# Optimization experiments

Hardware: AMD Instinct MI355X
Metric: run time of the kernel (lower is better)

Reference implementation:

```python
import jax, jax.numpy as jnp
import numpy as np

HID = 4096      # hidden_size
H = 32          # num_attention_heads
K = 8           # num_key_value_heads
D = HID // H    # head_dim = 128
G = H // K      # q heads per kv group = 4
INTER = 14336   # intermediate_size
T = 2048        # tokens (prefill)
EPS = 1e-5
THETA = 1000000.0


def setup_inputs() -> dict:
    key = jax.random.key(0)
    ks = jax.random.split(key, 9)
    s = 0.02
    return {
        "hidden_states": jax.random.normal(ks[0], (T, HID), jnp.float32),
        "position_ids": jnp.arange(T, dtype=jnp.int64),
        "wqkv": jax.random.normal(ks[1], ((H + 2 * K) * D, HID), jnp.float32) * s,
        "wo": jax.random.normal(ks[2], (HID, HID), jnp.float32) * s,
        "w1": jax.random.normal(ks[3], (INTER, HID), jnp.float32) * s,  # gate
        "w3": jax.random.normal(ks[4], (INTER, HID), jnp.float32) * s,  # up
        "w2": jax.random.normal(ks[5], (HID, INTER), jnp.float32) * s,  # down
        "attn_norm_w": jnp.ones((HID,), jnp.float32),
        "ffn_norm_w": jnp.ones((HID,), jnp.float32),
    }


def _rmsnorm(x, w):
    var = jnp.mean(jnp.square(x), axis=-1, keepdims=True)
    return x * jax.lax.rsqrt(var + EPS) * w


def _rope(x, cos, sin):
    # non-interleaved (half-split) rotation; x: [T, h, D], cos/sin: [T, 1, D//2]
    x1, x2 = x[..., : D // 2], x[..., D // 2 :]
    return jnp.concatenate([x1 * cos - x2 * sin, x2 * cos + x1 * sin], axis=-1)


def _attention(x, position_ids, wqkv, wo):
    t = x.shape[0]
    qkv = x @ wqkv.T  # [T, (H+2K)*D]
    q = qkv[:, : H * D].reshape(t, H, D)
    k = qkv[:, H * D : (H + K) * D].reshape(t, K, D)
    v = qkv[:, (H + K) * D :].reshape(t, K, D)

    inv_freq = 1.0 / (THETA ** (jnp.arange(0, D, 2, dtype=jnp.float32) / D))
    freqs = position_ids.astype(jnp.float32)[:, None] * inv_freq  # [T, D//2]
    cos = jnp.cos(freqs)[:, None, :]
    sin = jnp.sin(freqs)[:, None, :]
    q = _rope(q, cos, sin)
    k = _rope(k, cos, sin)

    # grouped-query attention: [T, K, G, D] queries vs [T, K, D] keys
    qg = q.reshape(t, K, G, D)
    scale = 1.0 / jnp.sqrt(jnp.float32(D))
    scores = jnp.einsum("tkgd,skd->kgts", qg, k) * scale  # [K, G, T, T]
    causal = jnp.tril(jnp.ones((t, t), dtype=bool))
    scores = jnp.where(causal, scores, jnp.finfo(scores.dtype).min)
    probs = jax.nn.softmax(scores, axis=-1)
    out = jnp.einsum("kgts,skd->tkgd", probs, v).reshape(t, H * D)
    return out @ wo.T


def _mlp(x, w1, w3, w2):
    return (jax.nn.silu(x @ w1.T) * (x @ w3.T)) @ w2.T


def reference(hidden_states, position_ids, wqkv, wo, w1, w3, w2, attn_norm_w, ffn_norm_w):
    h = hidden_states + _attention(_rmsnorm(hidden_states, attn_norm_w), position_ids, wqkv, wo)
    return h + _mlp(_rmsnorm(h, ffn_norm_w), w1, w3, w2)
```

## Files before the change

### kernel.cpp

```cpp
#include <hip/hip_runtime.h>
#include <stdint.h>

#define T_SEQ 2048
#define HIDN  4096
#define NH    32
#define NKV   8
#define DH    128
#define INTER 14336
#define QKV_N 6144
#define EPSR  1e-5f
#define SCALE 0.08838834764831845f

typedef __bf16 bf16x8 __attribute__((ext_vector_type(8)));
typedef float  f32x4  __attribute__((ext_vector_type(4)));

__device__ __forceinline__ f32x4 mfma16(bf16x8 a, bf16x8 b, f32x4 c) {
  return __builtin_amdgcn_mfma_f32_16x16x32_bf16(a, b, c, 0, 0, 0);
}

__device__ __forceinline__ void glds16(const void* g, void* l) {
  __builtin_amdgcn_global_load_lds(
      (__attribute__((address_space(1))) void*)g,
      (__attribute__((address_space(3))) void*)l,
      16, 0, 0);
}

__global__ __launch_bounds__(256) void cvt_bf16_kernel(
    const float* __restrict__ src, __bf16* __restrict__ dst, long n) {
  long stride = (long)gridDim.x * 256 * 8;
  for (long i = ((long)blockIdx.x * 256 + threadIdx.x) * 8; i < n; i += stride) {
    float4 a = *(const float4*)(src + i);
    float4 b = *(const float4*)(src + i + 4);
    bf16x8 o;
    o[0]=(__bf16)a.x; o[1]=(__bf16)a.y; o[2]=(__bf16)a.z; o[3]=(__bf16)a.w;
    o[4]=(__bf16)b.x; o[5]=(__bf16)b.y; o[6]=(__bf16)b.z; o[7]=(__bf16)b.w;
    *(bf16x8*)(dst + i) = o;
  }
}

__global__ __launch_bounds__(256) void rmsnorm_kernel(
    const float* __restrict__ x, const float* __restrict__ w,
    __bf16* __restrict__ y) {
  const int row = blockIdx.x, tid = threadIdx.x;
  const float* xr = x + (size_t)row * HIDN + tid * 16;
  float4 v0 = ((const float4*)xr)[0];
  float4 v1 = ((const float4*)xr)[1];
  float4 v2 = ((const float4*)xr)[2];
  float4 v3 = ((const float4*)xr)[3];
  float ss = v0.x*v0.x + v0.y*v0.y + v0.z*v0.z + v0.w*v0.w
           + v1.x*v1.x + v1.y*v1.y + v1.z*v1.z + v1.w*v1.w
           + v2.x*v2.x + v2.y*v2.y + v2.z*v2.z + v2.w*v2.w
           + v3.x*v3.x + v3.y*v3.y + v3.z*v3.z + v3.w*v3.w;
  #pragma unroll
  for (int off = 32; off >= 1; off >>= 1) ss += __shfl_xor(ss, off, 64);
  __shared__ float red[4];
  if ((tid & 63) == 0) red[tid >> 6] = ss;
  __syncthreads();
  float rn = rsqrtf((red[0] + red[1] + red[2] + red[3]) * (1.0f / HIDN) + EPSR);
  const float* wr = w + tid * 16;
  float4 w0 = ((const float4*)wr)[0];
  float4 w1v = ((const float4*)wr)[1];
  float4 w2v = ((const float4*)wr)[2];
  float4 w3v = ((const float4*)wr)[3];
  bf16x8 o0, o1;
  o0[0]=(__bf16)(v0.x*rn*w0.x);  o0[1]=(__bf16)(v0.y*rn*w0.y);
  o0[2]=(__bf16)(v0.z*rn*w0.z);  o0[3]=(__bf16)(v0.w*rn*w0.w);
  o0[4]=(__bf16)(v1.x*rn*w1v.x); o0[5]=(__bf16)(v1.y*rn*w1v.y);
  o0[6]=(__bf16)(v1.z*rn*w1v.z); o0[7]=(__bf16)(v1.w*rn*w1v.w);
  o1[0]=(__bf16)(v2.x*rn*w2v.x); o1[1]=(__bf16)(v2.y*rn*w2v.y);
  o1[2]=(__bf16)(v2.z*rn*w2v.z); o1[3]=(__bf16)(v2.w*rn*w2v.w);
  o1[4]=(__bf16)(v3.x*rn*w3v.x); o1[5]=(__bf16)(v3.y*rn*w3v.y);
  o1[6]=(__bf16)(v3.z*rn*w3v.z); o1[7]=(__bf16)(v3.w*rn*w3v.w);
  __bf16* yo = y + (size_t)row * HIDN + tid * 16;
  *(bf16x8*)(yo)     = o0;
  *(bf16x8*)(yo + 8) = o1;
}

template<int EPI>
__global__ __launch_bounds__(512, 2) void gemm256_kernel(
    const __bf16* __restrict__ A, const __bf16* __restrict__ B,
    void* __restrict__ Cout, int M, int N, int Kfull, int KZ) {
  extern __shared__ __align__(16) char smem[];
  const int tid = threadIdx.x;
  const int lane = tid & 63;
  const int wv = tid >> 6;
  const int wm = wv >> 2;
  const int wn = wv & 3;
  const int lr = lane & 15, q = lane >> 4;

  const int gx = gridDim.x, gy = gridDim.y;
  const int nwg = gx * gy;
  const int orig = blockIdx.y * gx + blockIdx.x;
  const int cpx = nwg >> 3;
  const int swz = (orig & 7) * cpx + (orig >> 3);
  const int by = swz % gy, bx = swz / gy;
  const int m0 = by * 256, n0 = bx * 256;
  const int kbase = blockIdx.z * KZ;
  const int NT = KZ >> 5;

  const char* aS[2]; const char* bS[2]; int Lds[2];
  #pragma unroll
  for (int j = 0; j < 2; j++) {
    int L = j * 512 + tid;
    int row = L >> 2;
    int s = (L & 3) ^ ((row >> 1) & 3);
    aS[j] = (const char*)(A + (size_t)(m0 + row) * Kfull + kbase + s * 8);
    bS[j] = (const char*)(B + (size_t)(n0 + row) * Kfull + kbase + s * 8);
    Lds[j] = L * 16;
  }

  const int sA = q ^ ((lr >> 1) & 3);
  int aoff[8], boff[4];
  #pragma unroll
  for (int mt = 0; mt < 8; mt++) aoff[mt] = (wm * 128 + mt * 16 + lr) * 64 + sA * 16;
  #pragma unroll
  for (int nt = 0; nt < 4; nt++) boff[nt] = 16384 + (wn * 64 + nt * 16 + lr) * 64 + sA * 16;

#define STAGE_T(tile, sb) do {                                   \
    char* _b = smem + (sb) * 32768;                              \
    size_t _ko = (size_t)(tile) * 64;                            \
    glds16(aS[0] + _ko, _b + Lds[0]);                            \
    glds16(aS[1] + _ko, _b + Lds[1]);                            \
    glds16(bS[0] + _ko, _b + 16384 + Lds[0]);                    \
    glds16(bS[1] + _ko, _b + 16384 + Lds[1]);                    \
  } while (0)

#define GBODY(VMC, DOST) do {                                    \
    if (DOST) { STAGE_T(t + 3, sbufi); sbufi = (sbufi == 4) ? 0 : sbufi + 1; } \
    asm volatile("s_waitcnt vmcnt(" #VMC ")" ::: "memory");      \
    __builtin_amdgcn_s_barrier();                                \
    asm volatile("" ::: "memory");                               \
    __builtin_amdgcn_sched_barrier(0);                           \
    { const char* _bA = smem + bufi * 32768;                     \
      bf16x8 bf[4], af[8];                                       \
      _Pragma("unroll") for (int nt = 0; nt < 4; nt++)           \
        bf[nt] = *(const bf16x8*)(_bA + boff[nt]);               \
      _Pragma("unroll") for (int mt = 0; mt < 8; mt++)           \
        af[mt] = *(const bf16x8*)(_bA + aoff[mt]);               \
      __builtin_amdgcn_s_setprio(1);                             \
      _Pragma("unroll") for (int mt = 0; mt < 8; mt++)           \
        _Pragma("unroll") for (int nt = 0; nt < 4; nt++)         \
          acc[mt][nt] = mfma16(af[mt], bf[nt], acc[mt][nt]);     \
      __builtin_amdgcn_s_setprio(0); }                           \
    bufi = (bufi == 4) ? 0 : bufi + 1;                           \
  } while (0)

  f32x4 acc[8][4] = {};
  STAGE_T(0, 0); STAGE_T(1, 1); STAGE_T(2, 2);
  int bufi = 0, sbufi = 3;
  for (int t = 0; t < NT - 3; ++t) GBODY(12, true);
  { int t = 0; (void)t;
    GBODY(8, false); GBODY(4, false); GBODY(0, false); }
#undef STAGE_T
#undef GBODY

  #pragma unroll
  for (int mt = 0; mt < 8; mt++) {
    #pragma unroll
    for (int r = 0; r < 4; r++) {
      int rr = m0 + wm * 128 + mt * 16 + q * 4 + r;
      #pragma unroll
      for (int nt = 0; nt < 4; nt++) {
        int cc = n0 + wn * 64 + nt * 16 + lr;
        size_t ix = (size_t)rr * N + cc;
        float val = acc[mt][nt][r];
        if (EPI == 0) ((float*)Cout)[(size_t)blockIdx.z * M * N + ix] = val;
        else          ((__bf16*)Cout)[ix] = (__bf16)val;
      }
    }
  }
}

__global__ __launch_bounds__(256) void add3_kernel(
    const float* __restrict__ p, const float* __restrict__ r,
    float* __restrict__ o, long n) {
  long stride = (long)gridDim.x * 1024;
  for (long i = ((long)blockIdx.x * 256 + threadIdx.x) * 4; i < n; i += stride) {
    float4 a = *(const float4*)(p + i);
    float4 b = *(const float4*)(p + n + i);
    float4 c = *(const float4*)(r + i);
    float4 o4;
    o4.x = a.x + b.x + c.x; o4.y = a.y + b.y + c.y;
    o4.z = a.z + b.z + c.z; o4.w = a.w + b.w + c.w;
    *(float4*)(o + i) = o4;
  }
}

__global__ __launch_bounds__(256) void rope_kernel(
    const __bf16* __restrict__ qkv, __bf16* __restrict__ q_r,
    __bf16* __restrict__ k_r) {
  const int t = blockIdx.x, tid = threadIdx.x;
  __shared__ float cs[64], sn[64];
  if (tid < 64) {
    float inv = exp2f(-(float)tid * (19.931568569324174f / 64.0f));
    float f = (float)t * inv;
    cs[tid] = cosf(f);
    sn[tid] = sinf(f);
  }
  __syncthreads();
  const __bf16* row = qkv + (size_t)t * QKV_N;
  for (int it = tid; it < 40 * 64; it += 256) {
    int hh = it >> 6, i = it & 63;
    float x1 = (float)row[hh * 128 + i];
    float x2 = (float)row[hh * 128 + 64 + i];
    float c = cs[i], s = sn[i];
    float o1 = x1 * c - x2 * s;
    float o2 = x2 * c + x1 * s;
    if (hh < NH) {
      __bf16* qo = q_r + (size_t)t * HIDN + hh * 128;
      qo[i] = (__bf16)o1;
      qo[64 + i] = (__bf16)o2;
    } else {
      __bf16* ko = k_r + (size_t)t * (NKV * DH) + (hh - NH) * 128;
      ko[i] = (__bf16)o1;
      ko[64 + i] = (__bf16)o2;
    }
  }
}

__global__ __launch_bounds__(256) void attn_kernel(
    const __bf16* __restrict__ q_r, const __bf16* __restrict__ k_r,
    const __bf16* __restrict__ qkv, __bf16* __restrict__ attn_o) {
  __shared__ __align__(16) __bf16 Ks[32 * 128];
  __shared__ __align__(16) __bf16 Vt[128][40];
  __shared__ __align__(16) __bf16 Pl[4][16][40];

  const int tid = threadIdx.x;
  const int lane = tid & 63, wv = tid >> 6;
  const int qt = blockIdx.x, h = blockIdx.y;
  const int kh = h >> 2;
  const int q0b = qt * 64;
  const int q0w = q0b + wv * 16;

  bf16x8 qf[4];
  {
    const __bf16* qp = q_r + (size_t)(q0w + (lane & 15)) * HIDN + h * DH + ((lane >> 4) << 3);
    #pragma unroll
    for (int kk = 0; kk < 4; kk++) qf[kk] = *(const bf16x8*)(qp + kk * 32);
  }

  f32x4 o[8] = {};
  float mrun[4] = {-1e30f, -1e30f, -1e30f, -1e30f};
  float lrun[4] = {0.f, 0.f, 0.f, 0.f};

  const int kv_end = q0b + 64;
  for (int kv0 = 0; kv0 < kv_end; kv0 += 32) {
    __syncthreads();
    #pragma unroll
    for (int i = 0; i < 2; i++) {
      int idx = i * 256 + tid;
      int row = idx >> 4;
      int cb = ((idx & 15) * 16) ^ ((row & 7) << 4);
      glds16((const char*)(k_r + (size_t)(kv0 + row) * (NKV * DH) + kh * DH) + cb,
             (char*)Ks + idx * 16);
    }
    {
      int d = tid & 127;
      int kvh = (tid >> 7) << 4;
      const __bf16* vp = qkv + (size_t)(kv0 + kvh) * QKV_N + (NH + NKV) * DH + kh * DH + d;
      #pragma unroll
      for (int j = 0; j < 16; j++) Vt[d][kvh + j] = vp[(size_t)j * QKV_N];
    }
    __syncthreads();

    if (q0w + 15 >= kv0) {
      f32x4 s[2] = {};
      #pragma unroll
      for (int kk = 0; kk < 4; kk++) {
        #pragma unroll
        for (int jt = 0; jt < 2; jt++) {
          int row = jt * 16 + (lane & 15);
          int cb = (kk * 64 + ((lane >> 4) << 4)) ^ ((row & 7) << 4);
          bf16x8 kf = *(const bf16x8*)((char*)Ks + row * 256 + cb);
          s[jt] = mfma16(qf[kk], kf, s[jt]);
        }
      }
      float p0[4], p1[4], mx[4];
      const bool need_mask = (kv0 + 31) > q0w;
      #pragma unroll
      for (int r = 0; r < 4; r++) {
        float a = s[0][r] * SCALE, b = s[1][r] * SCALE;
        if (need_mask) {
          int qpos = q0w + ((lane >> 4) << 2) + r;
          int kva = kv0 + (lane & 15);
          if (kva > qpos) a = -1e30f;
          if (kva + 16 > qpos) b = -1e30f;
        }
        p0[r] = a; p1[r] = b;
        mx[r] = fmaxf(a, b);
      }
      #pragma unroll
      for (int r = 0; r < 4; r++) {
        #pragma unroll
        for (int off = 1; off < 16; off <<= 1)
          mx[r] = fmaxf(mx[r], __shfl_xor(mx[r], off, 64));
        float mn = fmaxf(mrun[r], mx[r]);
        float corr = __expf(mrun[r] - mn);
        mrun[r] = mn;
        p0[r] = __expf(p0[r] - mn);
        p1[r] = __expf(p1[r] - mn);
        float ps = p0[r] + p1[r];
        #pragma unroll
        for (int off = 1; off < 16; off <<= 1) ps += __shfl_xor(ps, off, 64);
        lrun[r] = lrun[r] * corr + ps;
        #pragma unroll
        for (int nt = 0; nt < 8; nt++) o[nt][r] *= corr;
        int prow = ((lane >> 4) << 2) + r;
        Pl[wv][prow][lane & 15]      = (__bf16)p0[r];
        Pl[wv][prow][16 + (lane & 15)] = (__bf16)p1[r];
      }
      bf16x8 pf = *(const bf16x8*)&Pl[wv][lane & 15][(lane >> 4) << 3];
      #pragma unroll
      for (int nt = 0; nt < 8; nt++) {
        bf16x8 vf = *(const bf16x8*)&Vt[nt * 16 + (lane & 15)][(lane >> 4) << 3];
        o[nt] = mfma16(pf, vf, o[nt]);
      }
    }
  }

  #pragma unroll
  for (int nt = 0; nt < 8; nt++) {
    #pragma unroll
    for (int r = 0; r < 4; r++) {
      int qrow = q0w + ((lane >> 4) << 2) + r;
      int d = nt * 16 + (lane & 15);
      attn_o[(size_t)qrow * HIDN + h * DH + d] = (__bf16)(o[nt][r] / lrun[r]);
    }
  }
}

__global__ __launch_bounds__(256) void silu_mul_kernel(
    const __bf16* __restrict__ u, const __bf16* __restrict__ v,
    __bf16* __restrict__ g, long n) {
  long stride = (long)gridDim.x * 256 * 8;
  for (long i = ((long)blockIdx.x * 256 + threadIdx.x) * 8; i < n; i += stride) {
    bf16x8 uu = *(const bf16x8*)(u + i);
    bf16x8 vv = *(const bf16x8*)(v + i);
    bf16x8 gg;
    #pragma unroll
    for (int j = 0; j < 8; j++) {
      float x = (float)uu[j];
      float y = (float)vv[j];
      float sl = x / (1.0f + __expf(-x));
      gg[j] = (__bf16)(sl * y);
    }
    *(bf16x8*)(g + i) = gg;
  }
}

extern "C" void kernel_launch(void* const* d_in, const int* in_sizes, int n_in,
                              void* d_out, int out_size, void* d_ws, size_t ws_size,
                              hipStream_t stream) {
  const float* hidden = (const float*)d_in[0];
  const float* wqkv = (const float*)d_in[2];
  const float* wo   = (const float*)d_in[3];
  const float* w1   = (const float*)d_in[4];
  const float* w3   = (const float*)d_in[5];
  const float* w2   = (const float*)d_in[6];
  const float* anw  = (const float*)d_in[7];
  const float* fnw  = (const float*)d_in[8];

  char* ws = (char*)d_ws;
  const size_t SZ_XN   = (size_t)T_SEQ * HIDN * 2;
  const size_t SZ_QKV  = (size_t)T_SEQ * QKV_N * 2;
  const size_t SZ_KR   = (size_t)T_SEQ * NKV * DH * 2;
  const size_t SZ_H    = (size_t)T_SEQ * HIDN * 4;
  const size_t SZ_UV   = (size_t)T_SEQ * INTER * 2;

  const size_t W_QKV = (size_t)QKV_N * HIDN * 2;
  const size_t W_O   = (size_t)HIDN * HIDN * 2;
  const size_t W_I   = (size_t)INTER * HIDN * 2;
  const size_t W_TOTAL = W_QKV + W_O + 3 * W_I;

  char* act = ws + W_TOTAL;

  __bf16* xn1    = (__bf16*)(act);
  __bf16* qkv    = (__bf16*)(act + SZ_XN);
  __bf16* q_r    = (__bf16*)(act + SZ_XN + SZ_QKV);
  __bf16* ubuf   = (__bf16*)(act);
  __bf16* k_r    = (__bf16*)(act + SZ_UV);
  __bf16* attn_o = (__bf16*)(act + SZ_UV + SZ_KR);
  float*  hbuf   = (float*) (act + SZ_UV + SZ_KR + SZ_XN);
  __bf16* xn2    = (__bf16*)(act + SZ_UV + SZ_KR + SZ_XN + SZ_H);
  __bf16* vbuf   = (__bf16*)(act + SZ_UV + SZ_KR + SZ_XN + SZ_H + SZ_XN);
  __bf16* gbuf   = ubuf;
  float*  pbuf   = (float*)(act + SZ_UV + SZ_KR + SZ_XN + SZ_H);

  __bf16* wqkv_b = (__bf16*)(ws);
  __bf16* wo_b   = (__bf16*)(ws + W_QKV);
  __bf16* w1_b   = (__bf16*)(ws + W_QKV + W_O);
  __bf16* w3_b   = (__bf16*)(ws + W_QKV + W_O + W_I);
  __bf16* w2_b   = (__bf16*)(ws + W_QKV + W_O + 2 * W_I);

  const int LDS_BYTES = 163840;
  hipFuncSetAttribute((const void*)gemm256_kernel<0>,
                      hipFuncAttributeMaxDynamicSharedMemorySize, LDS_BYTES);
  hipFuncSetAttribute((const void*)gemm256_kernel<1>,
                      hipFuncAttributeMaxDynamicSharedMemorySize, LDS_BYTES);

  cvt_bf16_kernel<<<2048, 256, 0, stream>>>(wqkv, wqkv_b, (long)QKV_N * HIDN);
  cvt_bf16_kernel<<<2048, 256, 0, stream>>>(wo,   wo_b,   (long)HIDN * HIDN);
  cvt_bf16_kernel<<<2048, 256, 0, stream>>>(w1,   w1_b,   (long)INTER * HIDN);
  cvt_bf16_kernel<<<2048, 256, 0, stream>>>(w3,   w3_b,   (long)INTER * HIDN);
  cvt_bf16_kernel<<<2048, 256, 0, stream>>>(w2,   w2_b,   (long)HIDN * INTER);

  rmsnorm_kernel<<<T_SEQ, 256, 0, stream>>>(hidden, anw, xn1);
  gemm256_kernel<1><<<dim3(QKV_N / 256, T_SEQ / 256, 1), 512, LDS_BYTES, stream>>>(
      xn1, wqkv_b, qkv, T_SEQ, QKV_N, HIDN, HIDN);
  rope_kernel<<<T_SEQ, 256, 0, stream>>>(qkv, q_r, k_r);
  attn_kernel<<<dim3(T_SEQ / 64, NH), 256, 0, stream>>>(q_r, k_r, qkv, attn_o);
  gemm256_kernel<0><<<dim3(HIDN / 256, T_SEQ / 256, 2), 512, LDS_BYTES, stream>>>(
      attn_o, wo_b, pbuf, T_SEQ, HIDN, HIDN, HIDN / 2);
  add3_kernel<<<2048, 256, 0, stream>>>(pbuf, hidden, hbuf, (long)T_SEQ * HIDN);
  rmsnorm_kernel<<<T_SEQ, 256, 0, stream>>>(hbuf, fnw, xn2);
  gemm256_kernel<1><<<dim3(INTER / 256, T_SEQ / 256, 1), 512, LDS_BYTES, stream>>>(
      xn2, w1_b, ubuf, T_SEQ, INTER, HIDN, HIDN);
  gemm256_kernel<1><<<dim3(INTER / 256, T_SEQ / 256, 1), 512, LDS_BYTES, stream>>>(
      xn2, w3_b, vbuf, T_SEQ, INTER, HIDN, HIDN);
  silu_mul_kernel<<<2048, 256, 0, stream>>>(ubuf, vbuf, gbuf, (long)T_SEQ * INTER);
  gemm256_kernel<0><<<dim3(HIDN / 256, T_SEQ / 256, 2), 512, LDS_BYTES, stream>>>(
      gbuf, w2_b, pbuf, T_SEQ, HIDN, INTER, INTER / 2);
  add3_kernel<<<2048, 256, 0, stream>>>(pbuf, hbuf, (float*)d_out, (long)T_SEQ * HIDN);
}
```

Measured before the change: 1.414 ms.

## Pre-transpose V and widen attention KV tiles to 64 with async LDS loads

Adds a kernel that transposes V into a [kv_head][d][t] layout, so the attention kernel can stream V tiles into shared memory with asynchronous global-to-LDS loads instead of strided scalar gathers. The KV block size grows from 32 to 64, with XOR-swizzled K, V and P tiles to avoid bank conflicts. Query tiles are launched in reverse order so the longest causal blocks start first. This adds an extra launch and a V copy in the workspace, reusing the hbuf region before it is written.

```diff
diff --git a/kernel.cpp b/kernel.cpp
--- a/kernel.cpp
+++ b/kernel.cpp
@@ -10,6 +10,7 @@
 #define QKV_N 6144
 #define EPSR  1e-5f
 #define SCALE 0.08838834764831845f
+#define KVB   64
 
 typedef __bf16 bf16x8 __attribute__((ext_vector_type(8)));
 typedef float  f32x4  __attribute__((ext_vector_type(4)));
@@ -218,23 +219,49 @@
   }
 }
 
+__global__ __launch_bounds__(256) void vtrans_kernel(
+    const __bf16* __restrict__ qkv, __bf16* __restrict__ v_t) {
+  __shared__ __bf16 tile[64][136];
+  const int tid = threadIdx.x;
+  const int t0 = blockIdx.x * 64, kh = blockIdx.y;
+  #pragma unroll
+  for (int i = 0; i < 4; i++) {
+    int u = i * 256 + tid;
+    int row = u >> 4, c = (u & 15) * 8;
+    *(bf16x8*)&tile[row][c] =
+        *(const bf16x8*)(qkv + (size_t)(t0 + row) * QKV_N + (NH + NKV) * DH + kh * DH + c);
+  }
+  __syncthreads();
+  const int d = tid & 127, th = (tid >> 7) * 32;
+  #pragma unroll
+  for (int j = 0; j < 4; j++) {
+    int t = th + j * 8;
+    bf16x8 o;
+    #pragma unroll
+    for (int e = 0; e < 8; e++) o[e] = tile[t + e][d];
+    *(bf16x8*)(v_t + ((size_t)kh * DH + d) * T_SEQ + t0 + t) = o;
+  }
+}
+
 __global__ __launch_bounds__(256) void attn_kernel(
     const __bf16* __restrict__ q_r, const __bf16* __restrict__ k_r,
-    const __bf16* __restrict__ qkv, __bf16* __restrict__ attn_o) {
-  __shared__ __align__(16) __bf16 Ks[32 * 128];
-  __shared__ __align__(16) __bf16 Vt[128][40];
-  __shared__ __align__(16) __bf16 Pl[4][16][40];
+    const __bf16* __restrict__ v_t, __bf16* __restrict__ attn_o) {
+  __shared__ __align__(16) __bf16 Ks[KVB * 128];
+  __shared__ __align__(16) __bf16 Vs[128 * KVB];
+  __shared__ __align__(16) __bf16 Pl[4 * 16 * KVB];
 
   const int tid = threadIdx.x;
   const int lane = tid & 63, wv = tid >> 6;
-  const int qt = blockIdx.x, h = blockIdx.y;
+  const int lr = lane & 15, g = lane >> 4;
+  const int qt = gridDim.x - 1 - blockIdx.x;
+  const int h = blockIdx.y;
   const int kh = h >> 2;
   const int q0b = qt * 64;
   const int q0w = q0b + wv * 16;
 
   bf16x8 qf[4];
   {
-    const __bf16* qp = q_r + (size_t)(q0w + (lane & 15)) * HIDN + h * DH + ((lane >> 4) << 3);
+    const __bf16* qp = q_r + (size_t)(q0w + lr) * HIDN + h * DH + g * 8;
     #pragma unroll
     for (int kk = 0; kk < 4; kk++) qf[kk] = *(const bf16x8*)(qp + kk * 32);
   }
@@ -242,78 +269,85 @@
   f32x4 o[8] = {};
   float mrun[4] = {-1e30f, -1e30f, -1e30f, -1e30f};
   float lrun[4] = {0.f, 0.f, 0.f, 0.f};
-
-  const int kv_end = q0b + 64;
-  for (int kv0 = 0; kv0 < kv_end; kv0 += 32) {
+  char* PlW = (char*)Pl + wv * 2048;
+
+  for (int kv0 = 0; kv0 < q0b + KVB; kv0 += KVB) {
     __syncthreads();
     #pragma unroll
-    for (int i = 0; i < 2; i++) {
-      int idx = i * 256 + tid;
-      int row = idx >> 4;
-      int cb = ((idx & 15) * 16) ^ ((row & 7) << 4);
+    for (int i = 0; i < 4; i++) {
+      int u = i * 256 + tid;
+      int row = u >> 4;
+      int cb = ((u & 15) * 16) ^ ((row & 7) << 4);
       glds16((const char*)(k_r + (size_t)(kv0 + row) * (NKV * DH) + kh * DH) + cb,
-             (char*)Ks + idx * 16);
-    }
-    {
-      int d = tid & 127;
-      int kvh = (tid >> 7) << 4;
-      const __bf16* vp = qkv + (size_t)(kv0 + kvh) * QKV_N + (NH + NKV) * DH + kh * DH + d;
-      #pragma unroll
-      for (int j = 0; j < 16; j++) Vt[d][kvh + j] = vp[(size_t)j * QKV_N];
+             (char*)Ks + u * 16);
+    }
+    #pragma unroll
+    for (int i = 0; i < 4; i++) {
+      int u = i * 256 + tid;
+      int row = u >> 3;
+      int cb = ((u & 7) * 16) ^ ((row & 7) << 4);
+      glds16((const char*)(v_t + ((size_t)kh * DH + row) * T_SEQ + kv0) + cb,
+             (char*)Vs + u * 16);
     }
     __syncthreads();
 
     if (q0w + 15 >= kv0) {
-      f32x4 s[2] = {};
+      f32x4 s[4] = {};
       #pragma unroll
       for (int kk = 0; kk < 4; kk++) {
         #pragma unroll
-        for (int jt = 0; jt < 2; jt++) {
-          int row = jt * 16 + (lane & 15);
-          int cb = (kk * 64 + ((lane >> 4) << 4)) ^ ((row & 7) << 4);
-          bf16x8 kf = *(const bf16x8*)((char*)Ks + row * 256 + cb);
+        for (int jt = 0; jt < 4; jt++) {
+          int krow = jt * 16 + lr;
+          int cb = (kk * 64 + g * 16) ^ ((krow & 7) << 4);
+          bf16x8 kf = *(const bf16x8*)((char*)Ks + krow * 256 + cb);
           s[jt] = mfma16(qf[kk], kf, s[jt]);
         }
       }
-      float p0[4], p1[4], mx[4];
-      const bool need_mask = (kv0 + 31) > q0w;
+      const bool need_mask = (kv0 + KVB - 1) > q0w;
       #pragma unroll
       for (int r = 0; r < 4; r++) {
-        float a = s[0][r] * SCALE, b = s[1][r] * SCALE;
-        if (need_mask) {
-          int qpos = q0w + ((lane >> 4) << 2) + r;
-          int kva = kv0 + (lane & 15);
-          if (kva > qpos) a = -1e30f;
-          if (kva + 16 > qpos) b = -1e30f;
+        int qpos = q0w + g * 4 + r;
+        int prow = g * 4 + r;
+        float p[4];
+        #pragma unroll
+        for (int jt = 0; jt < 4; jt++) {
+          float v = s[jt][r] * SCALE;
+          if (need_mask && (kv0 + jt * 16 + lr > qpos)) v = -1e30f;
+          p[jt] = v;
         }
-        p0[r] = a; p1[r] = b;
-        mx[r] = fmaxf(a, b);
-      }
-      #pragma unroll
-      for (int r = 0; r < 4; r++) {
-        #pragma unroll
-        for (int off = 1; off < 16; off <<= 1)
-          mx[r] = fmaxf(mx[r], __shfl_xor(mx[r], off, 64));
-        float mn = fmaxf(mrun[r], mx[r]);
+        float mx = fmaxf(fmaxf(p[0], p[1]), fmaxf(p[2], p[3]));
+        #pragma unroll
+        for (int off = 1; off < 16; off <<= 1) mx = fmaxf(mx, __shfl_xor(mx, off, 64));
+        float mn = fmaxf(mrun[r], mx);
         float corr = __expf(mrun[r] - mn);
         mrun[r] = mn;
-        p0[r] = __expf(p0[r] - mn);
-        p1[r] = __expf(p1[r] - mn);
-        float ps = p0[r] + p1[r];
+        float ps = 0.f;
+        #pragma unroll
+        for (int jt = 0; jt < 4; jt++) {
+          p[jt] = __expf(p[jt] - mn);
+          ps += p[jt];
+          int cbyte = ((jt * 16 + lr) * 2) ^ ((prow & 7) << 4);
+          *(__bf16*)(PlW + prow * 128 + cbyte) = (__bf16)p[jt];
+        }
         #pragma unroll
         for (int off = 1; off < 16; off <<= 1) ps += __shfl_xor(ps, off, 64);
         lrun[r] = lrun[r] * corr + ps;
         #pragma unroll
         for (int nt = 0; nt < 8; nt++) o[nt][r] *= corr;
-        int prow = ((lane >> 4) << 2) + r;
-        Pl[wv][prow][lane & 15]      = (__bf16)p0[r];
-        Pl[wv][prow][16 + (lane & 15)] = (__bf16)p1[r];
       }
-      bf16x8 pf = *(const bf16x8*)&Pl[wv][lane & 15][(lane >> 4) << 3];
+      bf16x8 pa[2];
+      #pragma unroll
+      for (int ks = 0; ks < 2; ks++)
+        pa[ks] = *(const bf16x8*)(PlW + lr * 128 + ((g * 16 + ks * 64) ^ ((lr & 7) << 4)));
       #pragma unroll
       for (int nt = 0; nt < 8; nt++) {
-        bf16x8 vf = *(const bf16x8*)&Vt[nt * 16 + (lane & 15)][(lane >> 4) << 3];
-        o[nt] = mfma16(pf, vf, o[nt]);
+        #pragma unroll
+        for (int ks = 0; ks < 2; ks++) {
+          int vrow = nt * 16 + lr;
+          int cb = (ks * 64 + g * 16) ^ ((vrow & 7) << 4);
+          bf16x8 vf = *(const bf16x8*)((char*)Vs + vrow * 128 + cb);
+          o[nt] = mfma16(pa[ks], vf, o[nt]);
+        }
       }
     }
   }
@@ -322,8 +356,8 @@
   for (int nt = 0; nt < 8; nt++) {
     #pragma unroll
     for (int r = 0; r < 4; r++) {
-      int qrow = q0w + ((lane >> 4) << 2) + r;
-      int d = nt * 16 + (lane & 15);
+      int qrow = q0w + g * 4 + r;
+      int d = nt * 16 + lr;
       attn_o[(size_t)qrow * HIDN + h * DH + d] = (__bf16)(o[nt][r] / lrun[r]);
     }
   }
@@ -381,6 +415,7 @@
   __bf16* k_r    = (__bf16*)(act + SZ_UV);
   __bf16* attn_o = (__bf16*)(act + SZ_UV + SZ_KR);
   float*  hbuf   = (float*) (act + SZ_UV + SZ_KR + SZ_XN);
+  __bf16* v_t    = (__bf16*)(act + SZ_UV + SZ_KR + SZ_XN);
   __bf16* xn2    = (__bf16*)(act + SZ_UV + SZ_KR + SZ_XN + SZ_H);
   __bf16* vbuf   = (__bf16*)(act + SZ_UV + SZ_KR + SZ_XN + SZ_H + SZ_XN);
   __bf16* gbuf   = ubuf;
@@ -408,7 +443,8 @@
   gemm256_kernel<1><<<dim3(QKV_N / 256, T_SEQ / 256, 1), 512, LDS_BYTES, stream>>>(
       xn1, wqkv_b, qkv, T_SEQ, QKV_N, HIDN, HIDN);
   rope_kernel<<<T_SEQ, 256, 0, stream>>>(qkv, q_r, k_r);
-  attn_kernel<<<dim3(T_SEQ / 64, NH), 256, 0, stream>>>(q_r, k_r, qkv, attn_o);
+  vtrans_kernel<<<dim3(T_SEQ / 64, NKV), 256, 0, stream>>>(qkv, v_t);
+  attn_kernel<<<dim3(T_SEQ / 64, NH), 256, 0, stream>>>(q_r, k_r, v_t, attn_o);
   gemm256_kernel<0><<<dim3(HIDN / 256, T_SEQ / 256, 2), 512, LDS_BYTES, stream>>>(
       attn_o, wo_b, pbuf, T_SEQ, HIDN, HIDN, HIDN / 2);
   add3_kernel<<<2048, 256, 0, stream>>>(pbuf, hidden, hbuf, (long)T_SEQ * HIDN);
```

New measurement: 1.342 ms. -5.1%, faster.
